# Kernel tuning notes

Hardware: AMD Instinct MI355X
Metric: run time of the kernel (lower is better)

The kernel has to match this reference:

```python
import jax, jax.numpy as jnp
from jax import lax
import numpy as np

T, B = 64, 32            # rollout length, num envs
IMG = 84                 # NatureCNN input size
POS_N = 10               # grid size per position axis
N_ACT = 5                # discrete actions
HID = 128                # LSTM hidden size
CNN_OUT = 512
IN_DIM = CNN_OUT + 2 * POS_N  # 532


def setup_inputs() -> dict:
    key = jax.random.key(0)
    ks = jax.random.split(key, 16)
    N = T * B
    s = 0.05  # weight scale to keep activations in sane range
    rn = lambda k, shp: jax.random.normal(k, shp, jnp.float32) * s
    return {
        "image": jax.random.uniform(ks[0], (N, IMG, IMG, 3), jnp.float32),
        "position": jax.random.randint(ks[1], (N, 2), 0, POS_N, jnp.int32),
        "done": jax.random.randint(ks[2], (N,), 0, 2, jnp.int32),
        "h0": jnp.zeros((B, 1, HID), jnp.float32),
        "c0": jnp.zeros((B, 1, HID), jnp.float32),
        "W1": rn(ks[3], (8, 8, 3, 32)),   "b1": jnp.zeros((32,), jnp.float32),
        "W2": rn(ks[4], (4, 4, 32, 64)),  "b2": jnp.zeros((64,), jnp.float32),
        "W3": rn(ks[5], (3, 3, 64, 64)),  "b3": jnp.zeros((64,), jnp.float32),
        "Wfc": rn(ks[6], (3136, CNN_OUT)), "bfc": jnp.zeros((CNN_OUT,), jnp.float32),
        "Wih": rn(ks[7], (4 * HID, IN_DIM)), "Whh": rn(ks[8], (4 * HID, HID)),
        "bih": jnp.zeros((4 * HID,), jnp.float32), "bhh": jnp.zeros((4 * HID,), jnp.float32),
        "Wp": rn(ks[9], (HID, N_ACT)), "bp": jnp.zeros((N_ACT,), jnp.float32),
        "Wv": rn(ks[10], (HID, 1)),    "bv": jnp.zeros((1,), jnp.float32),
    }


def _conv(x, w, b, stride):
    y = lax.conv_general_dilated(x, w, (stride, stride), 'VALID',
                                 dimension_numbers=('NHWC', 'HWIO', 'NHWC'))
    return jax.nn.relu(y + b)


def reference(image, position, done, h0, c0,
              W1, b1, W2, b2, W3, b3, Wfc, bfc,
              Wih, Whh, bih, bhh, Wp, bp, Wv, bv):
    # --- NatureCNN feature extractor ---
    x = _conv(image, W1, b1, 4)          # (N,20,20,32)
    x = _conv(x, W2, b2, 2)              # (N,9,9,64)
    x = _conv(x, W3, b3, 1)              # (N,7,7,64)
    x = x.reshape(x.shape[0], -1)        # (N,3136)
    feat = jax.nn.relu(x @ Wfc + bfc)    # (N,512)
    # --- one-hot position encoding ---
    oh = jnp.concatenate([jax.nn.one_hot(position[:, 0], POS_N, dtype=feat.dtype),
                          jax.nn.one_hot(position[:, 1], POS_N, dtype=feat.dtype)], axis=1)
    z = jnp.concatenate([feat, oh], axis=1).reshape(T, B, IN_DIM)
    d = done.astype(feat.dtype).reshape(T, B)
    # --- per-timestep masked LSTM scan with episode resets ---
    h = h0[:, 0, :]  # (B,HID), num_layers=1
    c = c0[:, 0, :]

    def step(carry, inp):
        h, c = carry
        x_t, d_t = inp
        m = (1.0 - d_t)[:, None]
        h = h * m
        c = c * m
        g = x_t @ Wih.T + bih + h @ Whh.T + bhh          # (B,4*HID)
        i, f, gg, o = jnp.split(g, 4, axis=1)             # torch gate order i,f,g,o
        i = jax.nn.sigmoid(i)
        f = jax.nn.sigmoid(f)
        o = jax.nn.sigmoid(o)
        c = f * c + i * jnp.tanh(gg)
        h = o * jnp.tanh(c)
        return (h, c), h

    (h, c), hs = lax.scan(step, (h, c), (z, d))
    H = hs.reshape(T * B, HID)
    logits = H @ Wp + bp                 # (N, N_ACT) -> Categorical logits
    v = H @ Wv + bv                      # (N, 1)
    return logits, v, h[:, None, :], c[:, None, :]
```

## Files before the change

### kernel.cpp

```cpp
#include <hip/hip_runtime.h>

typedef unsigned short ushort_t;
typedef unsigned int uint_t;
typedef __attribute__((ext_vector_type(8))) short short8;
typedef __attribute__((ext_vector_type(4))) short short4v;
typedef __attribute__((ext_vector_type(4))) float floatx4;

__device__ __forceinline__ float bf2f(ushort_t u){
    union { uint_t i; float f; } c; c.i = ((uint_t)u) << 16; return c.f;
}
__device__ __forceinline__ ushort_t f2bf(float x){
    union { float f; uint_t i; } c; c.f = x;
    uint_t i = c.i;
    return (ushort_t)((i + 0x7fffu + ((i >> 16) & 1u)) >> 16);
}
__device__ __forceinline__ uint_t cvt2fast(float a, float b){
    union { float f; uint_t i; } ca, cb; ca.f = a; cb.f = b;
    uint_t ia = ca.i + 0x8000u, ib = cb.i + 0x8000u;
    return __builtin_amdgcn_perm(ib, ia, 0x07060302u);
}
__device__ __forceinline__ float relu_f(float x){ return fmaxf(x, 0.0f); }
__device__ __forceinline__ float sigmoid_f(float x){ return 1.0f / (1.0f + __expf(-x)); }

#define NT 2048
#define TT 64

__global__ __launch_bounds__(256) void prep_kernel(
    const float* __restrict__ Wih, ushort_t* __restrict__ Wihb)
{
    int i = blockIdx.x * 256 + threadIdx.x;
    int j = i >> 9, k = i & 511;
    Wihb[i] = f2bf(Wih[j * 532 + k]);
}

__global__ __launch_bounds__(256) void prep_convw_kernel(
    const float* __restrict__ W1, const float* __restrict__ W2,
    const float* __restrict__ W3, ushort_t* __restrict__ W1b,
    ushort_t* __restrict__ W2b, ushort_t* __restrict__ W3b)
{
    int i = blockIdx.x * 256 + threadIdx.x;
    if (i < 8192) {
        int ky = i >> 10, oc = (i >> 5) & 31, k = i & 31;
        float v = 0.0f;
        if (k < 24) { int kx = k / 3, ic = k % 3; v = W1[((ky * 8 + kx) * 3 + ic) * 32 + oc]; }
        W1b[i] = f2bf(v);
        return;
    }
    i -= 8192;
    if (i < 32768) {
        int kk = i >> 11, oc = (i >> 5) & 63, ic = i & 31;
        W2b[i] = f2bf(W2[(kk * 32 + ic) * 64 + oc]);
        return;
    }
    i -= 32768;
    if (i < 36864) {
        int p = i >> 12, oc = (i >> 6) & 63, ic = i & 63;
        W3b[i] = f2bf(W3[(p * 64 + ic) * 64 + oc]);
    }
}

__global__ __launch_bounds__(256) void wfct_kernel(
    const float* __restrict__ Wfc, ushort_t* __restrict__ WfcT)
{
    __shared__ ushort_t t_s[64][65];
    int kb = blockIdx.x % 49, jb = blockIdx.x / 49;
    int k0 = kb * 64, j0 = jb * 64;
    int jj = threadIdx.x & 63, i4 = threadIdx.x >> 6;
    for (int rr = i4; rr < 64; rr += 4)
        t_s[rr][jj] = f2bf(Wfc[(size_t)(k0 + rr) * 512 + j0 + jj]);
    __syncthreads();
    for (int rr = i4; rr < 64; rr += 4)
        WfcT[(size_t)(j0 + rr) * 3136 + k0 + jj] = t_s[jj][rr];
}

__global__ __launch_bounds__(256, 6) void convs_mfma(
    const float* __restrict__ img,
    const ushort_t* __restrict__ W1b, const float* __restrict__ b1,
    const ushort_t* __restrict__ W2b, const float* __restrict__ b2,
    const ushort_t* __restrict__ W3b, const float* __restrict__ b3,
    ushort_t* __restrict__ out3)
{
    __shared__ __align__(16) ushort_t smem[12800];

    int n = blockIdx.x, tid = threadIdx.x;
    int w = tid >> 6, lane = tid & 63;
    int r = lane & 15, q = lane >> 4;

    {
        short8 bf0[8], bf1[8];
        #pragma unroll
        for (int ky = 0; ky < 8; ky++) {
            bf0[ky] = *(const short8*)(W1b + (ky * 32 +      r) * 32 + q * 8);
            bf1[ky] = *(const short8*)(W1b + (ky * 32 + 16 + r) * 32 + q * 8);
        }
        float bb0 = b1[r], bb1 = b1[16 + r];
        const float* abase = img + (size_t)n * 21168;
        for (int t = w; t < 25; t += 4) {
            int pxa = t * 16 + r;
            int oy = pxa / 20, ox = pxa % 20;
            floatx4 acc0 = {0.f, 0.f, 0.f, 0.f}, acc1 = {0.f, 0.f, 0.f, 0.f};
            #pragma unroll
            for (int ky = 0; ky < 8; ky++) {
                short8 a = {0,0,0,0,0,0,0,0};
                if (q < 3) {
                    const float* p = abase + ((oy * 4 + ky) * 84 + ox * 4) * 3 + q * 8;
                    float4 f0 = *(const float4*)p;
                    float4 f1 = *(const float4*)(p + 4);
                    union { uint_t u[4]; short8 s; } pk;
                    pk.u[0] = cvt2fast(f0.x, f0.y);
                    pk.u[1] = cvt2fast(f0.z, f0.w);
                    pk.u[2] = cvt2fast(f1.x, f1.y);
                    pk.u[3] = cvt2fast(f1.z, f1.w);
                    a = pk.s;
                }
                acc0 = __builtin_amdgcn_mfma_f32_16x16x32_bf16(a, bf0[ky], acc0, 0, 0, 0);
                acc1 = __builtin_amdgcn_mfma_f32_16x16x32_bf16(a, bf1[ky], acc1, 0, 0, 0);
            }
            int pxs = t * 16 + q * 4;
            #pragma unroll
            for (int i = 0; i < 4; i++) {
                int px = pxs + i;
                int y = px / 20, x = px % 20;
                int base = (x & 1) * 6400 + (y * 10 + (x >> 1)) * 8 + (r & 7);
                smem[base + ((r >> 3)    ) * 1600] = f2bf(relu_f(acc0[i] + bb0));
                smem[base + (2 + (r >> 3)) * 1600] = f2bf(relu_f(acc1[i] + bb1));
            }
        }
    }
    __syncthreads();

    float accv[6][4];
    {
        int oct = w;
        short8 bfr[16];
        #pragma unroll
        for (int kk = 0; kk < 16; kk++)
            bfr[kk] = *(const short8*)(W2b + (kk * 64 + oct * 16 + r) * 32 + q * 8);
        #pragma unroll
        for (int t = 0; t < 6; t++) {
            int pxa = min(t * 16 + r, 80);
            int oy = pxa / 9, ox = pxa % 9;
            floatx4 acc = {0.f, 0.f, 0.f, 0.f};
            #pragma unroll
            for (int ky = 0; ky < 4; ky++) {
                #pragma unroll
                for (int kxh = 0; kxh < 2; kxh++) {
                    int pos = (oy * 2 + ky) * 10 + ox + kxh;
                    const ushort_t* pe = smem + q * 1600 + pos * 8;
                    short8 ae = *(const short8*)pe;
                    short8 ao = *(const short8*)(pe + 6400);
                    acc = __builtin_amdgcn_mfma_f32_16x16x32_bf16(ae, bfr[ky * 4 + kxh * 2],     acc, 0, 0, 0);
                    acc = __builtin_amdgcn_mfma_f32_16x16x32_bf16(ao, bfr[ky * 4 + kxh * 2 + 1], acc, 0, 0, 0);
                }
            }
            #pragma unroll
            for (int i = 0; i < 4; i++) accv[t][i] = acc[i];
        }
    }
    __syncthreads();
    {
        int oct = w;
        float bb = b2[oct * 16 + r];
        int kcb = (2 * oct + (r >> 3)) * 648 + (r & 7);
        #pragma unroll
        for (int t = 0; t < 6; t++) {
            #pragma unroll
            for (int i = 0; i < 4; i++) {
                int px = t * 16 + q * 4 + i;
                if (px < 81)
                    smem[kcb + px * 8] = f2bf(relu_f(accv[t][i] + bb));
            }
        }
    }
    __syncthreads();

    {
        int oct = w;
        short8 bfr[18];
        #pragma unroll
        for (int p = 0; p < 9; p++) {
            #pragma unroll
            for (int h = 0; h < 2; h++)
                bfr[p * 2 + h] = *(const short8*)(W3b + (p * 64 + oct * 16 + r) * 64 + h * 32 + q * 8);
        }
        float bb = b3[oct * 16 + r];
        for (int t = 0; t < 4; t++) {
            int pxa = min(t * 16 + r, 48);
            int oy = pxa / 7, ox = pxa % 7;
            floatx4 acc = {0.f, 0.f, 0.f, 0.f};
            #pragma unroll
            for (int ky = 0; ky < 3; ky++) {
                #pragma unroll
                for (int kx = 0; kx < 3; kx++) {
                    int qin = (oy + ky) * 9 + ox + kx;
                    const ushort_t* p0 = smem + q * 648 + qin * 8;
                    short8 a0 = *(const short8*)p0;
                    short8 a1 = *(const short8*)(p0 + 4 * 648);
                    acc = __builtin_amdgcn_mfma_f32_16x16x32_bf16(a0, bfr[(ky * 3 + kx) * 2],     acc, 0, 0, 0);
                    acc = __builtin_amdgcn_mfma_f32_16x16x32_bf16(a1, bfr[(ky * 3 + kx) * 2 + 1], acc, 0, 0, 0);
                }
            }
            #pragma unroll
            for (int i = 0; i < 4; i++) {
                int px = t * 16 + q * 4 + i;
                if (px < 49)
                    out3[(size_t)n * 3136 + px * 64 + oct * 16 + r] = f2bf(relu_f(acc[i] + bb));
            }
        }
    }
}

__global__ __launch_bounds__(256) void fc_mfma_kernel(
    const ushort_t* __restrict__ A, const ushort_t* __restrict__ BT,
    const float* __restrict__ bfc, ushort_t* __restrict__ feat)
{
    int mb = blockIdx.x & 63, nb = blockIdx.x >> 6;
    int tid = threadIdx.x;
    int w = tid >> 6, lane = tid & 63;
    int r = lane & 15, q = lane >> 4;
    int m0 = mb * 32 + (w & 1) * 16;
    int n0 = nb * 64 + (w >> 1) * 32;
    const ushort_t* arow  = A  + (size_t)(m0 + r) * 3136 + q * 8;
    const ushort_t* brow0 = BT + (size_t)(n0 + r) * 3136 + q * 8;
    const ushort_t* brow1 = BT + (size_t)(n0 + 16 + r) * 3136 + q * 8;
    floatx4 acc0 = {0.f, 0.f, 0.f, 0.f}, acc1 = {0.f, 0.f, 0.f, 0.f};
    short8 a  = *(const short8*)arow;
    short8 b0 = *(const short8*)brow0;
    short8 b1 = *(const short8*)brow1;
    for (int kk = 1; kk < 98; kk++) {
        short8 an  = *(const short8*)(arow  + kk * 32);
        short8 b0n = *(const short8*)(brow0 + kk * 32);
        short8 b1n = *(const short8*)(brow1 + kk * 32);
        acc0 = __builtin_amdgcn_mfma_f32_16x16x32_bf16(a, b0, acc0, 0, 0, 0);
        acc1 = __builtin_amdgcn_mfma_f32_16x16x32_bf16(a, b1, acc1, 0, 0, 0);
        a = an; b0 = b0n; b1 = b1n;
    }
    acc0 = __builtin_amdgcn_mfma_f32_16x16x32_bf16(a, b0, acc0, 0, 0, 0);
    acc1 = __builtin_amdgcn_mfma_f32_16x16x32_bf16(a, b1, acc1, 0, 0, 0);
    int c0 = n0 + r, c1 = n0 + 16 + r;
    float bb0 = bfc[c0], bb1 = bfc[c1];
    #pragma unroll
    for (int i = 0; i < 4; i++) {
        int row = m0 + q * 4 + i;
        feat[(size_t)row * 512 + c0] = f2bf(relu_f(acc0[i] + bb0));
        feat[(size_t)row * 512 + c1] = f2bf(relu_f(acc1[i] + bb1));
    }
}

__global__ __launch_bounds__(256) void gates_mfma_kernel(
    const ushort_t* __restrict__ A, const ushort_t* __restrict__ Wihb,
    const float* __restrict__ Wih, const float* __restrict__ bih,
    const float* __restrict__ bhh, const int* __restrict__ pos,
    float* __restrict__ gx)
{
    int mb = blockIdx.x & 63, nb = blockIdx.x >> 6;
    int tid = threadIdx.x;
    int w = tid >> 6, lane = tid & 63;
    int r = lane & 15, q = lane >> 4;
    int m0 = mb * 32 + (w & 1) * 16;
    int n0 = nb * 64 + (w >> 1) * 32;
    const ushort_t* arow  = A    + (size_t)(m0 + r) * 512 + q * 8;
    const ushort_t* brow0 = Wihb + (size_t)(n0 + r) * 512 + q * 8;
    const ushort_t* brow1 = Wihb + (size_t)(n0 + 16 + r) * 512 + q * 8;
    floatx4 acc0 = {0.f, 0.f, 0.f, 0.f}, acc1 = {0.f, 0.f, 0.f, 0.f};
    short8 a  = *(const short8*)arow;
    short8 b0 = *(const short8*)brow0;
    short8 b1 = *(const short8*)brow1;
    for (int kk = 1; kk < 16; kk++) {
        short8 an  = *(const short8*)(arow  + kk * 32);
        short8 b0n = *(const short8*)(brow0 + kk * 32);
        short8 b1n = *(const short8*)(brow1 + kk * 32);
        acc0 = __builtin_amdgcn_mfma_f32_16x16x32_bf16(a, b0, acc0, 0, 0, 0);
        acc1 = __builtin_amdgcn_mfma_f32_16x16x32_bf16(a, b1, acc1, 0, 0, 0);
        a = an; b0 = b0n; b1 = b1n;
    }
    acc0 = __builtin_amdgcn_mfma_f32_16x16x32_bf16(a, b0, acc0, 0, 0, 0);
    acc1 = __builtin_amdgcn_mfma_f32_16x16x32_bf16(a, b1, acc1, 0, 0, 0);
    int j0 = n0 + r, j1 = n0 + 16 + r;
    float bias0 = bih[j0] + bhh[j0];
    float bias1 = bih[j1] + bhh[j1];
    #pragma unroll
    for (int i = 0; i < 4; i++) {
        int row = m0 + q * 4 + i;
        int p0 = pos[2 * row], p1 = pos[2 * row + 1];
        float oh0 = Wih[(size_t)j0 * 532 + 512 + p0] + Wih[(size_t)j0 * 532 + 522 + p1];
        float oh1 = Wih[(size_t)j1 * 532 + 512 + p0] + Wih[(size_t)j1 * 532 + 522 + p1];
        gx[(size_t)row * 512 + j0] = acc0[i] + bias0 + oh0;
        gx[(size_t)row * 512 + j1] = acc1[i] + bias1 + oh1;
    }
}

__global__ __launch_bounds__(512, 2) void lstm_kernel(
    const float* __restrict__ gx, const float* __restrict__ Whh,
    const int* __restrict__ done, const float* __restrict__ h0,
    const float* __restrict__ c0, ushort_t* __restrict__ hs,
    float* __restrict__ out)
{
    __shared__ __align__(16) float h_s[128];
    __shared__ float gates_s[512];
    int b = blockIdx.x, tid = threadIdx.x;
    int g = tid >> 7, j = tid & 127;

    float w[128];
    const float* wr = Whh + (size_t)(g * 128 + j) * 128;
    #pragma unroll
    for (int k = 0; k < 128; k += 4) {
        float4 v = *(const float4*)(wr + k);
        w[k] = v.x; w[k + 1] = v.y; w[k + 2] = v.z; w[k + 3] = v.w;
    }
    float h = h0[b * 128 + j];
    float c = c0[b * 128 + j];
    const float* gxb = gx + (size_t)b * 512;

    for (int t = 0; t < TT; t++) {
        float m = 1.0f - (float)done[t * 32 + b];
        c *= m;
        if (g == 0) h_s[j] = h * m;
        __syncthreads();
        float acc = 0.0f;
        #pragma unroll
        for (int k = 0; k < 128; k += 4) {
            float4 hv = *(const float4*)&h_s[k];
            acc = fmaf(w[k], hv.x, acc);
            acc = fmaf(w[k + 1], hv.y, acc);
            acc = fmaf(w[k + 2], hv.z, acc);
            acc = fmaf(w[k + 3], hv.w, acc);
        }
        acc += gxb[(size_t)t * 32 * 512 + (g << 7) + j];
        gates_s[(g << 7) + j] = acc;
        __syncthreads();
        float iv = sigmoid_f(gates_s[j]);
        float fv = sigmoid_f(gates_s[128 + j]);
        float gv = tanhf(gates_s[256 + j]);
        float ov = sigmoid_f(gates_s[384 + j]);
        c = fv * c + iv * gv;
        h = ov * tanhf(c);
        if (g == 0) hs[((size_t)t * 32 + b) * 128 + j] = f2bf(h);
    }
    if (g == 0) {
        out[12288 + b * 128 + j] = h;
        out[16384 + b * 128 + j] = c;
    }
}

__global__ __launch_bounds__(256) void heads_kernel(
    const ushort_t* __restrict__ hs, const float* __restrict__ Wp,
    const float* __restrict__ bp, const float* __restrict__ Wv,
    const float* __restrict__ bv, float* __restrict__ out)
{
    int id = blockIdx.x * 256 + threadIdx.x;
    int n = id / 6, q = id % 6;
    const ushort_t* hrow = hs + (size_t)n * 128;
    if (q < 5) {
        float acc = bp[q];
        for (int k = 0; k < 128; k++) acc = fmaf(bf2f(hrow[k]), Wp[k * 5 + q], acc);
        out[n * 5 + q] = acc;
    } else {
        float acc = bv[0];
        for (int k = 0; k < 128; k++) acc = fmaf(bf2f(hrow[k]), Wv[k], acc);
        out[10240 + n] = acc;
    }
}

extern "C" void kernel_launch(void* const* d_in, const int* in_sizes, int n_in,
                              void* d_out, int out_size, void* d_ws, size_t ws_size,
                              hipStream_t stream) {
    const float* image = (const float*)d_in[0];
    const int*   pos   = (const int*)d_in[1];
    const int*   done  = (const int*)d_in[2];
    const float* h0    = (const float*)d_in[3];
    const float* c0    = (const float*)d_in[4];
    const float* W1    = (const float*)d_in[5];
    const float* b1    = (const float*)d_in[6];
    const float* W2    = (const float*)d_in[7];
    const float* b2    = (const float*)d_in[8];
    const float* W3    = (const float*)d_in[9];
    const float* b3    = (const float*)d_in[10];
    const float* Wfc   = (const float*)d_in[11];
    const float* bfc   = (const float*)d_in[12];
    const float* Wih   = (const float*)d_in[13];
    const float* Whh   = (const float*)d_in[14];
    const float* bih   = (const float*)d_in[15];
    const float* bhh   = (const float*)d_in[16];
    const float* Wp    = (const float*)d_in[17];
    const float* bp    = (const float*)d_in[18];
    const float* Wv    = (const float*)d_in[19];
    const float* bv    = (const float*)d_in[20];

    char* ws = (char*)d_ws;
    ushort_t* Wihb = (ushort_t*)(ws + 0);
    ushort_t* WfcT = (ushort_t*)(ws + 524288);
    ushort_t* W1b  = (ushort_t*)(ws + 3735552);
    ushort_t* W2b  = (ushort_t*)(ws + 3751936);
    ushort_t* W3b  = (ushort_t*)(ws + 3817472);
    ushort_t* out3 = (ushort_t*)(ws + 4194304);
    ushort_t* feat = (ushort_t*)(ws + 17039360);
    float*    gx   = (float*)(ws + 19136512);
    ushort_t* hs   = (ushort_t*)(ws + 23330816);

    float* out = (float*)d_out;

    prep_kernel<<<1024, 256, 0, stream>>>(Wih, Wihb);
    prep_convw_kernel<<<304, 256, 0, stream>>>(W1, W2, W3, W1b, W2b, W3b);
    wfct_kernel<<<392, 256, 0, stream>>>(Wfc, WfcT);
    convs_mfma<<<2048, 256, 0, stream>>>(image, W1b, b1, W2b, b2, W3b, b3, out3);
    fc_mfma_kernel<<<512, 256, 0, stream>>>(out3, WfcT, bfc, feat);
    gates_mfma_kernel<<<512, 256, 0, stream>>>(feat, Wihb, Wih, bih, bhh, pos, gx);
    lstm_kernel<<<32, 512, 0, stream>>>(gx, Whh, done, h0, c0, hs, out);
    heads_kernel<<<48, 256, 0, stream>>>(hs, Wp, bp, Wv, bv, out);
}
```

Before: 609.0 us.

## Split conv weight fragments into phases and pad LDS strides in fused conv kernel

Conv1 now gives each wave one 16-channel output slice over half the pixel tiles, instead of two slices over a quarter of the tiles. Conv2 and conv3 load weight fragments in halves or per-ky slices and keep accumulators across the phases. This cuts live registers for weight fragments, although the occupancy hint drops from 6 to 5. The shared-memory chunk strides are padded (1600 to 1608, 648 to 656) to reduce LDS bank conflicts. The trade-off is more accumulator state held live across phases and a slightly larger LDS footprint.

```diff
diff --git a/kernel.cpp b/kernel.cpp
--- a/kernel.cpp
+++ b/kernel.cpp
@@ -73,32 +73,31 @@
         WfcT[(size_t)(j0 + rr) * 3136 + k0 + jj] = t_s[jj][rr];
 }
 
-__global__ __launch_bounds__(256, 6) void convs_mfma(
+__global__ __launch_bounds__(256, 5) void convs_mfma(
     const float* __restrict__ img,
     const ushort_t* __restrict__ W1b, const float* __restrict__ b1,
     const ushort_t* __restrict__ W2b, const float* __restrict__ b2,
     const ushort_t* __restrict__ W3b, const float* __restrict__ b3,
     ushort_t* __restrict__ out3)
 {
-    __shared__ __align__(16) ushort_t smem[12800];
+    __shared__ __align__(16) ushort_t smem[12864];
 
     int n = blockIdx.x, tid = threadIdx.x;
     int w = tid >> 6, lane = tid & 63;
     int r = lane & 15, q = lane >> 4;
 
     {
-        short8 bf0[8], bf1[8];
-        #pragma unroll
-        for (int ky = 0; ky < 8; ky++) {
-            bf0[ky] = *(const short8*)(W1b + (ky * 32 +      r) * 32 + q * 8);
-            bf1[ky] = *(const short8*)(W1b + (ky * 32 + 16 + r) * 32 + q * 8);
-        }
-        float bb0 = b1[r], bb1 = b1[16 + r];
+        int oct = w & 1, ph = w >> 1;
+        short8 bw[8];
+        #pragma unroll
+        for (int ky = 0; ky < 8; ky++)
+            bw[ky] = *(const short8*)(W1b + (ky * 32 + oct * 16 + r) * 32 + q * 8);
+        float bb = b1[oct * 16 + r];
         const float* abase = img + (size_t)n * 21168;
-        for (int t = w; t < 25; t += 4) {
+        for (int t = ph; t < 25; t += 2) {
             int pxa = t * 16 + r;
             int oy = pxa / 20, ox = pxa % 20;
-            floatx4 acc0 = {0.f, 0.f, 0.f, 0.f}, acc1 = {0.f, 0.f, 0.f, 0.f};
+            floatx4 acc = {0.f, 0.f, 0.f, 0.f};
             #pragma unroll
             for (int ky = 0; ky < 8; ky++) {
                 short8 a = {0,0,0,0,0,0,0,0};
@@ -113,55 +112,62 @@
                     pk.u[3] = cvt2fast(f1.z, f1.w);
                     a = pk.s;
                 }
-                acc0 = __builtin_amdgcn_mfma_f32_16x16x32_bf16(a, bf0[ky], acc0, 0, 0, 0);
-                acc1 = __builtin_amdgcn_mfma_f32_16x16x32_bf16(a, bf1[ky], acc1, 0, 0, 0);
+                acc = __builtin_amdgcn_mfma_f32_16x16x32_bf16(a, bw[ky], acc, 0, 0, 0);
             }
             int pxs = t * 16 + q * 4;
             #pragma unroll
             for (int i = 0; i < 4; i++) {
                 int px = pxs + i;
                 int y = px / 20, x = px % 20;
-                int base = (x & 1) * 6400 + (y * 10 + (x >> 1)) * 8 + (r & 7);
-                smem[base + ((r >> 3)    ) * 1600] = f2bf(relu_f(acc0[i] + bb0));
-                smem[base + (2 + (r >> 3)) * 1600] = f2bf(relu_f(acc1[i] + bb1));
+                int chunk = (x & 1) * 4 + oct * 2 + (r >> 3);
+                smem[chunk * 1608 + (y * 10 + (x >> 1)) * 8 + (r & 7)] = f2bf(relu_f(acc[i] + bb));
             }
         }
     }
     __syncthreads();
 
     float accv[6][4];
+    #pragma unroll
+    for (int t = 0; t < 6; t++) {
+        #pragma unroll
+        for (int i = 0; i < 4; i++) accv[t][i] = 0.0f;
+    }
     {
         int oct = w;
-        short8 bfr[16];
-        #pragma unroll
-        for (int kk = 0; kk < 16; kk++)
-            bfr[kk] = *(const short8*)(W2b + (kk * 64 + oct * 16 + r) * 32 + q * 8);
-        #pragma unroll
-        for (int t = 0; t < 6; t++) {
-            int pxa = min(t * 16 + r, 80);
-            int oy = pxa / 9, ox = pxa % 9;
-            floatx4 acc = {0.f, 0.f, 0.f, 0.f};
-            #pragma unroll
-            for (int ky = 0; ky < 4; ky++) {
+        #pragma unroll
+        for (int half = 0; half < 2; half++) {
+            short8 bfr[8];
+            #pragma unroll
+            for (int kk2 = 0; kk2 < 8; kk2++)
+                bfr[kk2] = *(const short8*)(W2b + ((half * 8 + kk2) * 64 + oct * 16 + r) * 32 + q * 8);
+            #pragma unroll
+            for (int t = 0; t < 6; t++) {
+                int pxa = min(t * 16 + r, 80);
+                int oy = pxa / 9, ox = pxa % 9;
+                floatx4 acc = {accv[t][0], accv[t][1], accv[t][2], accv[t][3]};
                 #pragma unroll
-                for (int kxh = 0; kxh < 2; kxh++) {
-                    int pos = (oy * 2 + ky) * 10 + ox + kxh;
-                    const ushort_t* pe = smem + q * 1600 + pos * 8;
-                    short8 ae = *(const short8*)pe;
-                    short8 ao = *(const short8*)(pe + 6400);
-                    acc = __builtin_amdgcn_mfma_f32_16x16x32_bf16(ae, bfr[ky * 4 + kxh * 2],     acc, 0, 0, 0);
-                    acc = __builtin_amdgcn_mfma_f32_16x16x32_bf16(ao, bfr[ky * 4 + kxh * 2 + 1], acc, 0, 0, 0);
+                for (int ky2 = 0; ky2 < 2; ky2++) {
+                    int ky = half * 2 + ky2;
+                    #pragma unroll
+                    for (int kxh = 0; kxh < 2; kxh++) {
+                        int pos = (oy * 2 + ky) * 10 + ox + kxh;
+                        const ushort_t* pe = smem + q * 1608 + pos * 8;
+                        short8 ae = *(const short8*)pe;
+                        short8 ao = *(const short8*)(pe + 4 * 1608);
+                        acc = __builtin_amdgcn_mfma_f32_16x16x32_bf16(ae, bfr[ky2 * 4 + kxh * 2],     acc, 0, 0, 0);
+                        acc = __builtin_amdgcn_mfma_f32_16x16x32_bf16(ao, bfr[ky2 * 4 + kxh * 2 + 1], acc, 0, 0, 0);
+                    }
                 }
-            }
-            #pragma unroll
-            for (int i = 0; i < 4; i++) accv[t][i] = acc[i];
+                #pragma unroll
+                for (int i = 0; i < 4; i++) accv[t][i] = acc[i];
+            }
         }
     }
     __syncthreads();
     {
         int oct = w;
         float bb = b2[oct * 16 + r];
-        int kcb = (2 * oct + (r >> 3)) * 648 + (r & 7);
+        int kcb = (oct * 2 + (r >> 3)) * 656 + (r & 7);
         #pragma unroll
         for (int t = 0; t < 6; t++) {
             #pragma unroll
@@ -176,35 +182,47 @@
 
     {
         int oct = w;
-        short8 bfr[18];
-        #pragma unroll
-        for (int p = 0; p < 9; p++) {
-            #pragma unroll
-            for (int h = 0; h < 2; h++)
-                bfr[p * 2 + h] = *(const short8*)(W3b + (p * 64 + oct * 16 + r) * 64 + h * 32 + q * 8);
-        }
-        float bb = b3[oct * 16 + r];
+        float acct[4][4];
+        #pragma unroll
         for (int t = 0; t < 4; t++) {
-            int pxa = min(t * 16 + r, 48);
-            int oy = pxa / 7, ox = pxa % 7;
-            floatx4 acc = {0.f, 0.f, 0.f, 0.f};
-            #pragma unroll
-            for (int ky = 0; ky < 3; ky++) {
+            #pragma unroll
+            for (int i = 0; i < 4; i++) acct[t][i] = 0.0f;
+        }
+        #pragma unroll
+        for (int ky = 0; ky < 3; ky++) {
+            short8 bfr[6];
+            #pragma unroll
+            for (int kx = 0; kx < 3; kx++) {
+                #pragma unroll
+                for (int h = 0; h < 2; h++)
+                    bfr[kx * 2 + h] = *(const short8*)(W3b + ((ky * 3 + kx) * 64 + oct * 16 + r) * 64 + h * 32 + q * 8);
+            }
+            #pragma unroll
+            for (int t = 0; t < 4; t++) {
+                int pxa = min(t * 16 + r, 48);
+                int oy = pxa / 7, ox = pxa % 7;
+                floatx4 acc = {acct[t][0], acct[t][1], acct[t][2], acct[t][3]};
                 #pragma unroll
                 for (int kx = 0; kx < 3; kx++) {
                     int qin = (oy + ky) * 9 + ox + kx;
-                    const ushort_t* p0 = smem + q * 648 + qin * 8;
+                    const ushort_t* p0 = smem + q * 656 + qin * 8;
                     short8 a0 = *(const short8*)p0;
-                    short8 a1 = *(const short8*)(p0 + 4 * 648);
-                    acc = __builtin_amdgcn_mfma_f32_16x16x32_bf16(a0, bfr[(ky * 3 + kx) * 2],     acc, 0, 0, 0);
-                    acc = __builtin_amdgcn_mfma_f32_16x16x32_bf16(a1, bfr[(ky * 3 + kx) * 2 + 1], acc, 0, 0, 0);
+                    short8 a1 = *(const short8*)(p0 + 4 * 656);
+                    acc = __builtin_amdgcn_mfma_f32_16x16x32_bf16(a0, bfr[kx * 2],     acc, 0, 0, 0);
+                    acc = __builtin_amdgcn_mfma_f32_16x16x32_bf16(a1, bfr[kx * 2 + 1], acc, 0, 0, 0);
                 }
-            }
+                #pragma unroll
+                for (int i = 0; i < 4; i++) acct[t][i] = acc[i];
+            }
+        }
+        float bb = b3[oct * 16 + r];
+        #pragma unroll
+        for (int t = 0; t < 4; t++) {
             #pragma unroll
             for (int i = 0; i < 4; i++) {
                 int px = t * 16 + q * 4 + i;
                 if (px < 49)
-                    out3[(size_t)n * 3136 + px * 64 + oct * 16 + r] = f2bf(relu_f(acc[i] + bb));
+                    out3[(size_t)n * 3136 + px * 64 + oct * 16 + r] = f2bf(relu_f(acct[t][i] + bb));
             }
         }
     }
```

Measured after the change: 584.8 us. 4.0% less time.
